# Kernel optimization log

Hardware: AMD Instinct MI355X
Metric: run time of the kernel (lower is better)

## Reference

```python
import jax, jax.numpy as jnp
import numpy as np

B, T, D = 4, 4096, 1024
H, K, V = 16, 64, 64
EPS = 1e-6


def setup_inputs() -> dict:
    key = jax.random.key(0)
    ks = jax.random.split(key, 7)
    s = 0.02
    return {
        "x": jax.random.normal(ks[0], (B, T, D), dtype=jnp.float32),
        "norm_w": jnp.ones((D,), dtype=jnp.float32),
        "Wk": jax.random.normal(ks[1], (H * K, D), dtype=jnp.float32) * s,
        "Wv": jax.random.normal(ks[2], (H * V, D), dtype=jnp.float32) * s,
        "Wo": jax.random.normal(ks[3], (D, H * V), dtype=jnp.float32) * s,
        "Wb": jax.random.normal(ks[4], (H, D), dtype=jnp.float32) * s,
        "bb": jnp.full((H,), -2.0, dtype=jnp.float32),
        "Wg": jax.random.normal(ks[5], (H, D), dtype=jnp.float32) * s,
        "bg": jnp.full((H,), 2.0, dtype=jnp.float32),
    }


def reference(x, norm_w, Wk, Wv, Wo, Wb, bb, Wg, bg):
    # RMSNorm
    rms = jnp.sqrt(jnp.mean(x * x, axis=-1, keepdims=True) + EPS)
    xn = x / rms * norm_w  # [B,T,D]

    k = (xn @ Wk.T).reshape(B, T, H, K)
    v = (xn @ Wv.T).reshape(B, T, H, V)
    # L2-normalize keys (F.normalize, eps=1e-12)
    kn = jnp.linalg.norm(k, axis=-1, keepdims=True)
    k = k / jnp.maximum(kn, 1e-12)

    beta = jax.nn.sigmoid(xn @ Wb.T + bb)  # [B,T,H]
    g = jax.nn.sigmoid(xn @ Wg.T + bg)     # [B,T,H]

    # time-major for scan
    k_t = jnp.transpose(k, (1, 0, 2, 3))       # [T,B,H,K]
    v_t = jnpp = jnp.transpose(v, (1, 0, 2, 3))  # [T,B,H,V]
    b_t = jnp.transpose(beta, (1, 0, 2))       # [T,B,H]
    g_t = jnp.transpose(g, (1, 0, 2))          # [T,B,H]

    state0 = jnp.zeros((B, H, K, V), dtype=jnp.float32)

    def step(state, inp):
        kt, vt, bt, gt = inp  # [B,H,K],[B,H,V],[B,H],[B,H]
        pred = jnp.einsum('bhkv,bhk->bhv', state, kt)
        err = vt - pred
        state = gt[..., None, None] * state + bt[..., None, None] * (kt[..., :, None] * err[..., None, :])
        out_t = jnp.einsum('bhkv,bhk->bhv', state, kt)
        return state, out_t

    final_state, out = jax.lax.scan(step, state0, (k_t, v_t, b_t, g_t))
    out = jnp.transpose(out, (1, 0, 2, 3)).reshape(B, T, H * V)  # [B,T,H*V]
    y = x + out @ Wo.T
    return y
```

## Files before the change

kernel.cpp:

```cpp
#include <hip/hip_runtime.h>
#include <stdint.h>

#define B_ 4
#define T_ 4096
#define D_ 1024
#define H_ 16
#define NPAD 2304
#define ROWS (B_*T_)

typedef __bf16 bf16x8 __attribute__((ext_vector_type(8)));
typedef float  f32x4  __attribute__((ext_vector_type(4)));
typedef unsigned short u16;
typedef u16 u16x8 __attribute__((ext_vector_type(8)));
typedef u16 u16x4 __attribute__((ext_vector_type(4)));

__device__ __forceinline__ float bf2f(u16 u){
  union { unsigned int i; float f; } x; x.i = ((unsigned int)u) << 16; return x.f;
}
__device__ __forceinline__ u16 f2bf(float f){
  union { float f; unsigned int i; } x; x.f = f;
  unsigned int r = x.i + 0x7fffu + ((x.i >> 16) & 1u);
  return (u16)(r >> 16);
}
__device__ __forceinline__ bf16x8 as_bf(u16x8 v){ union{u16x8 u; bf16x8 b;} x; x.u = v; return x.b; }

__device__ __forceinline__ void gload_lds16(const u16* g, u16* l){
  __builtin_amdgcn_global_load_lds(
      (const __attribute__((address_space(1))) unsigned int*)g,
      (__attribute__((address_space(3))) unsigned int*)l, 16, 0, 0);
}

__global__ __launch_bounds__(256) void prep_w(
    const float* __restrict__ Wk, const float* __restrict__ Wv,
    const float* __restrict__ Wb, const float* __restrict__ Wg,
    const float* __restrict__ Wo, u16* __restrict__ Wcomb, u16* __restrict__ Wob)
{
  long i = (long)blockIdx.x * 256 + threadIdx.x;
  const long tot1 = (long)NPAD * D_;
  if (i < tot1) {
    long n = i >> 10, d = i & 1023;
    float v;
    if      (n < 1024) v = Wk[n * 1024 + d];
    else if (n < 2048) v = Wv[(n - 1024) * 1024 + d];
    else if (n < 2064) v = Wb[(n - 2048) * 1024 + d];
    else if (n < 2080) v = Wg[(n - 2064) * 1024 + d];
    else               v = 0.f;
    Wcomb[i] = f2bf(v);
  } else {
    long j = i - tot1;
    Wob[j] = f2bf(Wo[j]);
  }
}

__global__ __launch_bounds__(256) void rmsnorm_k(
    const float* __restrict__ x, const float* __restrict__ w, u16* __restrict__ xn)
{
  long row = blockIdx.x;
  int tid = threadIdx.x;
  int l = tid & 63, wv = tid >> 6;
  f32x4 v = ((const f32x4*)(x + row * D_))[tid];
  float ss = v[0]*v[0] + v[1]*v[1] + v[2]*v[2] + v[3]*v[3];
  #pragma unroll
  for (int m = 1; m < 64; m <<= 1) ss += __shfl_xor(ss, m, 64);
  __shared__ float red[4];
  if (l == 0) red[wv] = ss;
  __syncthreads();
  float tot = red[0] + red[1] + red[2] + red[3];
  float inv = rsqrtf(tot * (1.f / (float)D_) + 1e-6f);
  f32x4 wv4 = ((const f32x4*)w)[tid];
  u16x4 o;
  o[0] = f2bf(v[0] * inv * wv4[0]);
  o[1] = f2bf(v[1] * inv * wv4[1]);
  o[2] = f2bf(v[2] * inv * wv4[2]);
  o[3] = f2bf(v[3] * inv * wv4[3]);
  ((u16x4*)(xn + row * D_))[tid] = o;
}

extern __shared__ f32x4 lds_dyn[];

template<int RESID, int OUTF32>
__global__ __launch_bounds__(512, 2) void gemm256(
    const u16* __restrict__ A, const u16* __restrict__ Bm,
    u16* __restrict__ Cb, float* __restrict__ Cf, const float* __restrict__ resid,
    int M, int N, int Kd)
{
  const int tid = threadIdx.x;
  const int w = tid >> 6, l = tid & 63;
  const int lm = l & 15, lq = l >> 4;
  const int wm = w >> 2, wn = w & 3;

  unsigned gx = gridDim.x;
  unsigned bid = blockIdx.y * gx + blockIdx.x;
  unsigned nwg = gx * gridDim.y;
  unsigned cpx = nwg >> 3;
  unsigned swz = (bid & 7) * cpx + (bid >> 3);
  const long bm0 = (long)(swz / gx) * 256;
  const long bn0 = (long)(swz % gx) * 256;

  char* lds = (char*)lds_dyn;

  int rowS[2], colS[2];
  #pragma unroll
  for (int r = 0; r < 2; ++r) {
    int c = r*512 + w*64 + l;
    int row = c >> 2, slot = c & 3;
    rowS[r] = row;
    colS[r] = (slot ^ (row & 3)) * 8;
  }

  auto STAGE_A = [&](int t, int q){
    char* base = lds + q*32768;
    long k0 = (long)t * 32;
    #pragma unroll
    for (int r = 0; r < 2; ++r)
      gload_lds16(A + (bm0 + rowS[r])*(long)Kd + k0 + colS[r],
                  (u16*)(base + (r*512 + w*64)*16));
  };
  auto STAGE_B = [&](int t, int q){
    char* base = lds + q*32768 + 16384;
    long k0 = (long)t * 32;
    #pragma unroll
    for (int r = 0; r < 2; ++r)
      gload_lds16(Bm + (bn0 + rowS[r])*(long)Kd + k0 + colS[r],
                  (u16*)(base + (r*512 + w*64)*16));
  };

  f32x4 acc[8][4];
  #pragma unroll
  for (int i = 0; i < 8; ++i)
    #pragma unroll
    for (int j = 0; j < 4; ++j) acc[i][j] = f32x4{0.f,0.f,0.f,0.f};

  const int NT = Kd >> 5;
  STAGE_A(0, 0); STAGE_B(0, 0);
  STAGE_A(1, 1); STAGE_B(1, 1);

  for (int t = 0; t < NT; ++t) {
    int q  = t % 3;
    int qn = (t + 2) % 3;
    int tn = (t + 2 < NT) ? (t + 2) : (NT - 1);

    asm volatile("s_waitcnt vmcnt(4)" ::: "memory");
    __builtin_amdgcn_s_barrier();
    asm volatile("" ::: "memory");

    const char* Ab = lds + q*32768;
    const char* Bb = Ab + 16384;

    bf16x8 bfr[4];
    #pragma unroll
    for (int nf = 0; nf < 4; ++nf) {
      int rr = wn*64 + nf*16 + lm;
      bfr[nf] = *(const bf16x8*)(Bb + rr*64 + (((unsigned)lq << 4) ^ ((unsigned)(rr & 3) << 4)));
    }
    bf16x8 afr[4];
    #pragma unroll
    for (int mf = 0; mf < 4; ++mf) {
      int rr = wm*128 + mf*16 + lm;
      afr[mf] = *(const bf16x8*)(Ab + rr*64 + (((unsigned)lq << 4) ^ ((unsigned)(rr & 3) << 4)));
    }
    STAGE_A(tn, qn);

    __builtin_amdgcn_s_setprio(1);
    #pragma unroll
    for (int mf = 0; mf < 4; ++mf)
      #pragma unroll
      for (int nf = 0; nf < 4; ++nf)
        acc[mf][nf] = __builtin_amdgcn_mfma_f32_16x16x32_bf16(afr[mf], bfr[nf], acc[mf][nf], 0, 0, 0);
    __builtin_amdgcn_s_setprio(0);

    __builtin_amdgcn_s_barrier();
    asm volatile("" ::: "memory");

    #pragma unroll
    for (int mf = 0; mf < 4; ++mf) {
      int rr = wm*128 + 64 + mf*16 + lm;
      afr[mf] = *(const bf16x8*)(Ab + rr*64 + (((unsigned)lq << 4) ^ ((unsigned)(rr & 3) << 4)));
    }
    STAGE_B(tn, qn);

    __builtin_amdgcn_s_setprio(1);
    #pragma unroll
    for (int mf = 0; mf < 4; ++mf)
      #pragma unroll
      for (int nf = 0; nf < 4; ++nf)
        acc[4+mf][nf] = __builtin_amdgcn_mfma_f32_16x16x32_bf16(afr[mf], bfr[nf], acc[4+mf][nf], 0, 0, 0);
    __builtin_amdgcn_s_setprio(0);
  }

  #pragma unroll
  for (int mf = 0; mf < 8; ++mf) {
    #pragma unroll
    for (int r = 0; r < 4; ++r) {
      long m = bm0 + wm*128 + mf*16 + lq*4 + r;
      #pragma unroll
      for (int nf = 0; nf < 4; ++nf) {
        long n = bn0 + wn*64 + nf*16 + lm;
        float val = acc[mf][nf][r];
        if (RESID) val += resid[m * N + n];
        if (OUTF32) Cf[m * N + n] = val;
        else        Cb[m * N + n] = f2bf(val);
      }
    }
  }
}

template<int RESID, int OUTF32>
__global__ __launch_bounds__(256) void gemm_nt(
    const u16* __restrict__ A, const u16* __restrict__ Bm,
    u16* __restrict__ Cb, float* __restrict__ Cf, const float* __restrict__ resid,
    int M, int N, int Kd)
{
  __shared__ __align__(16) u16 Als[128 * 32];
  __shared__ __align__(16) u16 Bls[128 * 32];
  const int tid = threadIdx.x;
  const int w = tid >> 6, l = tid & 63;
  const int wr = w >> 1, wc = w & 1;
  const int lm = l & 15, lq = l >> 4;

  unsigned bid = blockIdx.y * gridDim.x + blockIdx.x;
  unsigned nwg = gridDim.x * gridDim.y;
  unsigned cpx = nwg >> 3;
  unsigned swz = (bid & 7) * cpx + (bid >> 3);
  const long bm0 = (long)(swz / gridDim.x) * 128;
  const long bn0 = (long)(swz % gridDim.x) * 128;

  f32x4 zero4 = {0.f, 0.f, 0.f, 0.f};
  f32x4 acc[4][4];
  #pragma unroll
  for (int i = 0; i < 4; i++)
    #pragma unroll
    for (int j = 0; j < 4; j++) acc[i][j] = zero4;

  for (int kk = 0; kk < Kd; kk += 32) {
    __syncthreads();
    #pragma unroll
    for (int it = 0; it < 2; it++) {
      int c = tid + it * 256;
      int r = c >> 2, kb = c & 3;
      const u16* ga = A  + (bm0 + r) * Kd + kk + kb * 8;
      const u16* gb = Bm + (bn0 + r) * Kd + kk + kb * 8;
      gload_lds16(ga, Als + (it * 256 + w * 64) * 8);
      gload_lds16(gb, Bls + (it * 256 + w * 64) * 8);
    }
    __syncthreads();
    bf16x8 af[4], bfr[4];
    #pragma unroll
    for (int f = 0; f < 4; f++)
      af[f] = *(const bf16x8*)(Als + (wr * 64 + f * 16 + lm) * 32 + lq * 8);
    #pragma unroll
    for (int f = 0; f < 4; f++)
      bfr[f] = *(const bf16x8*)(Bls + (wc * 64 + f * 16 + lm) * 32 + lq * 8);
    #pragma unroll
    for (int i = 0; i < 4; i++)
      #pragma unroll
      for (int j = 0; j < 4; j++)
        acc[i][j] = __builtin_amdgcn_mfma_f32_16x16x32_bf16(af[i], bfr[j], acc[i][j], 0, 0, 0);
  }

  #pragma unroll
  for (int i = 0; i < 4; i++) {
    #pragma unroll
    for (int r = 0; r < 4; r++) {
      long m = bm0 + wr * 64 + i * 16 + lq * 4 + r;
      #pragma unroll
      for (int j = 0; j < 4; j++) {
        long n = bn0 + wc * 64 + j * 16 + lm;
        float val = acc[i][j][r];
        if (RESID) val += resid[m * N + n];
        if (OUTF32) Cf[m * N + n] = val;
        else        Cb[m * N + n] = f2bf(val);
      }
    }
  }
}

__global__ __launch_bounds__(64) void postproc(
    u16* __restrict__ kv, const float* __restrict__ bb, const float* __restrict__ bg,
    float* __restrict__ bArr, float* __restrict__ gArr)
{
  long row = blockIdx.x;
  int l = threadIdx.x;
  u16* rp = kv + row * NPAD;
  #pragma unroll
  for (int h = 0; h < 16; h++) {
    float xk = bf2f(rp[h * 64 + l]);
    float ss = xk * xk;
    #pragma unroll
    for (int m = 1; m < 64; m <<= 1) ss += __shfl_xor(ss, m, 64);
    float inv = 1.f / fmaxf(sqrtf(ss), 1e-12f);
    rp[h * 64 + l] = f2bf(xk * inv);
  }
  if (l < 32) {
    int hh = l & 15;
    float val = bf2f(rp[2048 + l]) + ((l < 16) ? bb[hh] : bg[hh]);
    float s = 1.f / (1.f + expf(-val));
    float* dst = (l < 16) ? bArr : gArr;
    long b = row >> 12;
    long t = row & 4095;
    dst[(b * H_ + hh) * (long)T_ + t] = s;
  }
}

__device__ __forceinline__ void mm64(const u16* Ab, const u16* Bb,
                                     int lm, int lq, int wr, int wc, f32x4 acc[2][2])
{
  #pragma unroll
  for (int ks = 0; ks < 2; ++ks) {
    bf16x8 af[2], bfr[2];
    #pragma unroll
    for (int mi = 0; mi < 2; ++mi)
      af[mi] = *(const bf16x8*)(Ab + (wr*32 + mi*16 + lm)*72 + ks*32 + lq*8);
    #pragma unroll
    for (int ni = 0; ni < 2; ++ni)
      bfr[ni] = *(const bf16x8*)(Bb + (wc*32 + ni*16 + lm)*72 + ks*32 + lq*8);
    #pragma unroll
    for (int mi = 0; mi < 2; ++mi)
      #pragma unroll
      for (int ni = 0; ni < 2; ++ni)
        acc[mi][ni] = __builtin_amdgcn_mfma_f32_16x16x32_bf16(af[mi], bfr[ni], acc[mi][ni], 0, 0, 0);
  }
}

__global__ __launch_bounds__(256) void chunk1(
    u16* __restrict__ kv, const float* __restrict__ bArr, const float* __restrict__ gArr,
    u16* __restrict__ p1buf, u16* __restrict__ r1buf)
{
  __shared__ __align__(16) u16 Kb[64*72];
  __shared__ __align__(16) u16 Utb[128*72];
  __shared__ __align__(16) u16 LpI[64*72];
  __shared__ __align__(16) u16 Abf[64*72];
  __shared__ __align__(16) float Ad[4*16*21];
  __shared__ float aLS[64], ainvLS[64], bLS[64], bapLS[64];
  __shared__ float aCsh;

  const int tid = threadIdx.x;
  const int w = tid >> 6, l = tid & 63;
  const int lm = l & 15, lq = l >> 4;
  const int wr = w >> 1, wc = w & 1;
  const int bh = blockIdx.x & 63, ch = blockIdx.x >> 6;
  const int b = bh >> 4, h = bh & 15;

  const u16* kbase = kv + ((long)b*T_ + ch*64)*NPAD + h*64;
  const u16* vbase = kbase + 1024;

  #pragma unroll
  for (int it = 0; it < 2; ++it) {
    int c = tid + it*256;
    int r = c >> 3, seg = (c & 7)*8;
    *(u16x8*)(Kb  + r*72 + seg) = *(const u16x8*)(kbase + (long)r*NPAD + seg);
    *(u16x8*)(Utb + r*72 + seg) = *(const u16x8*)(vbase + (long)r*NPAD + seg);
  }
  #pragma unroll
  for (int z = 0; z < 8; ++z) {
    int idx = tid + z*256;
    int rr = idx >> 5, wd = idx & 31;
    ((unsigned int*)(Utb + (64 + rr)*72))[wd] = 0u;
  }
  if (tid < 64) {
    float gv = gArr[(long)bh*T_ + ch*64 + tid];
    float bv = bArr[(long)bh*T_ + ch*64 + tid];
    float av = gv;
    #pragma unroll
    for (int off = 1; off < 64; off <<= 1) {
      float o = __shfl_up(av, off, 64);
      if (tid >= off) av *= o;
    }
    float ap = __shfl_up(av, 1, 64);
    if (tid == 0) ap = 1.f;
    float aC = __shfl(av, 63, 64);
    aLS[tid] = av; ainvLS[tid] = 1.f/av; bLS[tid] = bv; bapLS[tid] = bv*ap;
    if (tid == 0) aCsh = aC;
  }
  __syncthreads();

  f32x4 gf[2][2];
  #pragma unroll
  for (int mi = 0; mi < 2; ++mi)
    #pragma unroll
    for (int ni = 0; ni < 2; ++ni) gf[mi][ni] = f32x4{0.f,0.f,0.f,0.f};
  mm64(Kb, Kb, lm, lq, wr, wc, gf);

  float wv_[4][2][4];
  #pragma unroll
  for (int bi = 0; bi < 4; ++bi)
    #pragma unroll
    for (int ni = 0; ni < 2; ++ni) {
      int col = w*32 + ni*16 + lm;
      #pragma unroll
      for (int r = 0; r < 4; ++r) {
        int row = bi*16 + lq*4 + r;
        float sv = (col < 64) ? bf2f(Utb[row*72 + col]) : bf2f(Kb[row*72 + (col - 64)]);
        float coef = (col < 64) ? bLS[row] : bapLS[row];
        wv_[bi][ni][r] = coef * sv;
      }
    }

  #pragma unroll
  for (int mi = 0; mi < 2; ++mi)
    #pragma unroll
    for (int ni = 0; ni < 2; ++ni)
      #pragma unroll
      for (int r = 0; r < 4; ++r) {
        int row = wr*32 + mi*16 + lq*4 + r, col = wc*32 + ni*16 + lm;
        float gvl = gf[mi][ni][r];
        int rb = row >> 4, cb = col >> 4;
        Abf[row*72 + col] = f2bf((rb > cb) ? bapLS[row]*ainvLS[col]*gvl : 0.f);
        if (rb == cb)
          Ad[(rb*16 + (row & 15))*21 + (col & 15)] =
              ((col & 15) < (row & 15)) ? bapLS[row]*ainvLS[col]*gvl : 0.f;
        LpI[row*72 + col] = f2bf((col < row) ? aLS[row]*ainvLS[col]*gvl
                                             : ((col == row) ? 1.f : 0.f));
      }
  __syncthreads();

  #pragma unroll
  for (int bi = 0; bi < 4; ++bi) {
    if (bi > 0) {
      f32x4 corr[2] = { f32x4{0.f,0.f,0.f,0.f}, f32x4{0.f,0.f,0.f,0.f} };
      const int nks = (bi*16 + 31) >> 5;
      #pragma unroll
      for (int ks = 0; ks < 2; ++ks) {
        if (ks < nks) {
          bf16x8 afr = *(const bf16x8*)(Abf + (bi*16 + lm)*72 + ks*32 + lq*8);
          #pragma unroll
          for (int ni = 0; ni < 2; ++ni) {
            bf16x8 bfr = *(const bf16x8*)(Utb + (w*32 + ni*16 + lm)*72 + ks*32 + lq*8);
            corr[ni] = __builtin_amdgcn_mfma_f32_16x16x32_bf16(afr, bfr, corr[ni], 0, 0, 0);
          }
        }
      }
      #pragma unroll
      for (int ni = 0; ni < 2; ++ni)
        #pragma unroll
        for (int r = 0; r < 4; ++r) wv_[bi][ni][r] -= corr[ni][r];
    }
    #pragma unroll
    for (int i = 0; i < 16; ++i) {
      int src = ((i >> 2) << 4) | lm;
      float u0 = __shfl(wv_[bi][0][i & 3], src, 64);
      float u1 = __shfl(wv_[bi][1][i & 3], src, 64);
      #pragma unroll
      for (int r = 0; r < 4; ++r) {
        float ad = Ad[(bi*16 + lq*4 + r)*21 + i];
        wv_[bi][0][r] = fmaf(-ad, u0, wv_[bi][0][r]);
        wv_[bi][1][r] = fmaf(-ad, u1, wv_[bi][1][r]);
      }
    }
    #pragma unroll
    for (int ni = 0; ni < 2; ++ni) {
      int col = w*32 + ni*16 + lm;
      #pragma unroll
      for (int r = 0; r < 4; ++r)
        Utb[col*72 + bi*16 + lq*4 + r] = f2bf(wv_[bi][ni][r]);
    }
  }
  __syncthreads();

  const long pr_base = (((long)bh*64 + ch)*64);
  u16* qdst = kv + ((long)b*T_ + ch*64)*NPAD + h*64;
  u16* mdst = qdst + 1024;
  f32x4 acc[2][2];

  #pragma unroll
  for (int mi = 0; mi < 2; ++mi)
    #pragma unroll
    for (int ni = 0; ni < 2; ++ni) acc[mi][ni] = f32x4{0.f,0.f,0.f,0.f};
  mm64(Utb, LpI, lm, lq, wr, wc, acc);
  #pragma unroll
  for (int mi = 0; mi < 2; ++mi)
    #pragma unroll
    for (int ni = 0; ni < 2; ++ni)
      #pragma unroll
      for (int r = 0; r < 4; ++r) {
        int row = wr*32 + mi*16 + lq*4 + r, col = wc*32 + ni*16 + lm;
        p1buf[(pr_base + row)*64 + col] = f2bf(acc[mi][ni][r]);
      }

  #pragma unroll
  for (int mi = 0; mi < 2; ++mi)
    #pragma unroll
    for (int ni = 0; ni < 2; ++ni) acc[mi][ni] = f32x4{0.f,0.f,0.f,0.f};
  mm64(LpI, Utb + 64*72, lm, lq, wr, wc, acc);
  #pragma unroll
  for (int mi = 0; mi < 2; ++mi)
    #pragma unroll
    for (int ni = 0; ni < 2; ++ni)
      #pragma unroll
      for (int r = 0; r < 4; ++r) {
        int row = wr*32 + mi*16 + lq*4 + r, col = wc*32 + ni*16 + lm;
        float val = aLS[row]*bf2f(Kb[row*72 + col]) - acc[mi][ni][r];
        qdst[(long)row*NPAD + col] = f2bf(val);
      }

  {
    int kk_ = tid >> 2, sb = (tid & 3) * 16;
    float aC = aCsh;
    #pragma unroll
    for (int s5 = 0; s5 < 16; ++s5) {
      int s = sb + s5;
      Abf[kk_*72 + s] = f2bf(aC * ainvLS[s] * bf2f(Kb[s*72 + kk_]));
    }
  }
  __syncthreads();

  #pragma unroll
  for (int mi = 0; mi < 2; ++mi)
    #pragma unroll
    for (int ni = 0; ni < 2; ++ni) acc[mi][ni] = f32x4{0.f,0.f,0.f,0.f};
  mm64(Utb, Abf, lm, lq, wr, wc, acc);
  #pragma unroll
  for (int mi = 0; mi < 2; ++mi)
    #pragma unroll
    for (int ni = 0; ni < 2; ++ni)
      #pragma unroll
      for (int r = 0; r < 4; ++r) {
        int row = wr*32 + mi*16 + lq*4 + r, col = wc*32 + ni*16 + lm;
        r1buf[(pr_base + row)*64 + col] = f2bf(acc[mi][ni][r]);
      }

  #pragma unroll
  for (int mi = 0; mi < 2; ++mi)
    #pragma unroll
    for (int ni = 0; ni < 2; ++ni) acc[mi][ni] = f32x4{0.f,0.f,0.f,0.f};
  mm64(Abf, Utb + 64*72, lm, lq, wr, wc, acc);
  #pragma unroll
  for (int mi = 0; mi < 2; ++mi)
    #pragma unroll
    for (int ni = 0; ni < 2; ++ni)
      #pragma unroll
      for (int r = 0; r < 4; ++r) {
        int row = wr*32 + mi*16 + lq*4 + r, col = wc*32 + ni*16 + lm;
        float val = ((row == col) ? aCsh : 0.f) - acc[mi][ni][r];
        mdst[(long)row*NPAD + col] = f2bf(val);
      }
}

struct PF { u16x8 qf0, qf1, mf0, mf1; u16 p1[4]; u16 r1[4]; };

__global__ __launch_bounds__(256) void chunk2(
    const u16* __restrict__ kv, const u16* __restrict__ p1buf, const u16* __restrict__ r1buf,
    u16* __restrict__ outb)
{
  __shared__ __align__(16) u16 Zb[16*72];
  __shared__ __align__(16) u16 ot[64*24];
  const int tid = threadIdx.x;
  const int wcv = tid >> 6, l = tid & 63;
  const int lm = l & 15, lq = l >> 4;
  const int bh = blockIdx.x & 63, vg = blockIdx.x >> 6;
  const int b = bh >> 4, h = bh & 15;

  for (int idx = tid; idx < 16*72/2; idx += 256) ((unsigned int*)Zb)[idx] = 0u;

  const u16* pbase = p1buf + (long)bh*64*4096;
  const u16* rbase = r1buf + (long)bh*64*4096;

  auto LOADPF = [&](int ch, PF& p){
    long rq = ((long)b*T_ + ch*64 + wcv*16 + lm)*NPAD + h*64 + lq*8;
    p.qf0 = *(const u16x8*)(kv + rq);
    p.qf1 = *(const u16x8*)(kv + rq + 32);
    p.mf0 = *(const u16x8*)(kv + rq + 1024);
    p.mf1 = *(const u16x8*)(kv + rq + 1024 + 32);
    #pragma unroll
    for (int r = 0; r < 4; ++r) {
      long pv = (long)ch*4096 + (vg*16 + lq*4 + r)*64 + wcv*16 + lm;
      p.p1[r] = pbase[pv];
      p.r1[r] = rbase[pv];
    }
  };

  PF A, Bp;
  LOADPF(0, A);
  __syncthreads();

  auto STEP = [&](int ch, PF& use, PF& pre){
    bf16x8 za0 = *(const bf16x8*)(Zb + lm*72 + lq*8);
    bf16x8 za1 = *(const bf16x8*)(Zb + lm*72 + 32 + lq*8);
    if (ch < 63) LOADPF(ch + 1, pre);
    f32x4 accO = { bf2f(use.p1[0]), bf2f(use.p1[1]), bf2f(use.p1[2]), bf2f(use.p1[3]) };
    accO = __builtin_amdgcn_mfma_f32_16x16x32_bf16(za0, as_bf(use.qf0), accO, 0, 0, 0);
    accO = __builtin_amdgcn_mfma_f32_16x16x32_bf16(za1, as_bf(use.qf1), accO, 0, 0, 0);
    f32x4 accS = { bf2f(use.r1[0]), bf2f(use.r1[1]), bf2f(use.r1[2]), bf2f(use.r1[3]) };
    accS = __builtin_amdgcn_mfma_f32_16x16x32_bf16(za0, as_bf(use.mf0), accS, 0, 0, 0);
    accS = __builtin_amdgcn_mfma_f32_16x16x32_bf16(za1, as_bf(use.mf1), accS, 0, 0, 0);
    #pragma unroll
    for (int r = 0; r < 4; ++r) ot[(wcv*16 + lm)*24 + lq*4 + r] = f2bf(accO[r]);
    __syncthreads();
    #pragma unroll
    for (int r = 0; r < 4; ++r) Zb[(lq*4 + r)*72 + wcv*16 + lm] = f2bf(accS[r]);
    {
      int i2 = tid >> 2, q4 = tid & 3;
      u16x4 ov = *(const u16x4*)(ot + i2*24 + q4*4);
      *(u16x4*)(outb + ((long)b*T_ + ch*64 + i2)*D_ + h*64 + vg*16 + q4*4) = ov;
    }
    __syncthreads();
  };

  for (int c2 = 0; c2 < 32; ++c2) {
    STEP(2*c2,     A, Bp);
    STEP(2*c2 + 1, Bp, A);
  }
}

extern "C" void kernel_launch(void* const* d_in, const int* in_sizes, int n_in,
                              void* d_out, int out_size, void* d_ws, size_t ws_size,
                              hipStream_t stream) {
  const float* x     = (const float*)d_in[0];
  const float* normw = (const float*)d_in[1];
  const float* Wk    = (const float*)d_in[2];
  const float* Wv    = (const float*)d_in[3];
  const float* Wo    = (const float*)d_in[4];
  const float* Wb    = (const float*)d_in[5];
  const float* bb    = (const float*)d_in[6];
  const float* Wg    = (const float*)d_in[7];
  const float* bg    = (const float*)d_in[8];
  float* y = (float*)d_out;

  char* ws = (char*)d_ws;
  u16* xn    = (u16*)ws;   ws += (long)ROWS * D_ * 2;
  u16* Wcomb = (u16*)ws;   ws += (long)NPAD * D_ * 2;
  u16* Wob   = (u16*)ws;   ws += (long)D_ * D_ * 2;
  u16* kvb   = (u16*)ws;   ws += (long)ROWS * NPAD * 2;
  float* bA  = (float*)ws; ws += (long)B_ * H_ * T_ * 4;
  float* gA  = (float*)ws; ws += (long)B_ * H_ * T_ * 4;
  u16* outb  = (u16*)ws;   ws += (long)ROWS * D_ * 2;
  u16* r1b   = (u16*)ws;   ws += (long)64 * 64 * 4096 * 2;

  const int LDSB = 3 * 32768;
  bool big = true;
  if (hipFuncSetAttribute(reinterpret_cast<const void*>(gemm256<0,0>),
        hipFuncAttributeMaxDynamicSharedMemorySize, LDSB) != hipSuccess) big = false;
  if (hipFuncSetAttribute(reinterpret_cast<const void*>(gemm256<1,1>),
        hipFuncAttributeMaxDynamicSharedMemorySize, LDSB) != hipSuccess) big = false;

  const long prep_total = (long)NPAD * D_ + (long)D_ * D_;
  prep_w<<<dim3((unsigned)(prep_total / 256)), dim3(256), 0, stream>>>(
      Wk, Wv, Wb, Wg, Wo, Wcomb, Wob);
  rmsnorm_k<<<dim3(ROWS), dim3(256), 0, stream>>>(x, normw, xn);
  if (big)
    gemm256<0, 0><<<dim3(NPAD / 256, ROWS / 256), dim3(512), LDSB, stream>>>(
        xn, Wcomb, kvb, (float*)nullptr, (const float*)nullptr, ROWS, NPAD, D_);
  else
    gemm_nt<0, 0><<<dim3(NPAD / 128, ROWS / 128), dim3(256), 0, stream>>>(
        xn, Wcomb, kvb, (float*)nullptr, (const float*)nullptr, ROWS, NPAD, D_);
  postproc<<<dim3(ROWS), dim3(64), 0, stream>>>(kvb, bb, bg, bA, gA);
  chunk1<<<dim3(4096), dim3(256), 0, stream>>>(kvb, bA, gA, xn, r1b);
  chunk2<<<dim3(256), dim3(256), 0, stream>>>(kvb, xn, r1b, outb);
  if (big)
    gemm256<1, 1><<<dim3(D_ / 256, ROWS / 256), dim3(512), LDSB, stream>>>(
        outb, Wob, (u16*)nullptr, y, x, ROWS, D_, D_);
  else
    gemm_nt<1, 1><<<dim3(D_ / 128, ROWS / 128), dim3(256), 0, stream>>>(
        outb, Wob, (u16*)nullptr, y, x, ROWS, D_, D_);
}
```

Measured before the change: 348.8 us.

## Change LDS swizzle pattern and merge GEMM inner loop halves into one phase

The GEMM main loop now loads all 8 A fragments at once and issues both A and B prefetches before a single block of 32 MFMAs, removing the mid-iteration barrier. The LDS XOR swizzle changes to key on (row>>1)&3 instead of row&3, to cut bank conflicts on 16-byte fragment reads. This trades more live registers for fewer barriers, and the triple-buffer safety now rests on the one remaining barrier per iteration.

```diff
diff --git a/kernel.cpp b/kernel.cpp
--- a/kernel.cpp
+++ b/kernel.cpp
@@ -99,21 +99,17 @@
 
   char* lds = (char*)lds_dyn;
 
-  int rowS[2], colS[2];
-  #pragma unroll
-  for (int r = 0; r < 2; ++r) {
-    int c = r*512 + w*64 + l;
-    int row = c >> 2, slot = c & 3;
-    rowS[r] = row;
-    colS[r] = (slot ^ (row & 3)) * 8;
-  }
+  int rowS[2];
+  #pragma unroll
+  for (int r = 0; r < 2; ++r) rowS[r] = r*128 + w*16 + (l >> 2);
+  const int colS = ((l & 3) ^ ((l >> 3) & 3)) * 8;
 
   auto STAGE_A = [&](int t, int q){
     char* base = lds + q*32768;
     long k0 = (long)t * 32;
     #pragma unroll
     for (int r = 0; r < 2; ++r)
-      gload_lds16(A + (bm0 + rowS[r])*(long)Kd + k0 + colS[r],
+      gload_lds16(A + (bm0 + rowS[r])*(long)Kd + k0 + colS,
                   (u16*)(base + (r*512 + w*64)*16));
   };
   auto STAGE_B = [&](int t, int q){
@@ -121,9 +117,11 @@
     long k0 = (long)t * 32;
     #pragma unroll
     for (int r = 0; r < 2; ++r)
-      gload_lds16(Bm + (bn0 + rowS[r])*(long)Kd + k0 + colS[r],
+      gload_lds16(Bm + (bn0 + rowS[r])*(long)Kd + k0 + colS,
                   (u16*)(base + (r*512 + w*64)*16));
   };
+
+  const unsigned soff = (unsigned)(lq ^ ((lm >> 1) & 3)) << 4;
 
   f32x4 acc[8][4];
   #pragma unroll
@@ -147,44 +145,26 @@
     const char* Ab = lds + q*32768;
     const char* Bb = Ab + 16384;
 
-    bf16x8 bfr[4];
+    bf16x8 bfr[4], afr[8];
     #pragma unroll
     for (int nf = 0; nf < 4; ++nf) {
       int rr = wn*64 + nf*16 + lm;
-      bfr[nf] = *(const bf16x8*)(Bb + rr*64 + (((unsigned)lq << 4) ^ ((unsigned)(rr & 3) << 4)));
-    }
-    bf16x8 afr[4];
-    #pragma unroll
-    for (int mf = 0; mf < 4; ++mf) {
+      bfr[nf] = *(const bf16x8*)(Bb + rr*64 + soff);
+    }
+    #pragma unroll
+    for (int mf = 0; mf < 8; ++mf) {
       int rr = wm*128 + mf*16 + lm;
-      afr[mf] = *(const bf16x8*)(Ab + rr*64 + (((unsigned)lq << 4) ^ ((unsigned)(rr & 3) << 4)));
+      afr[mf] = *(const bf16x8*)(Ab + rr*64 + soff);
     }
     STAGE_A(tn, qn);
+    STAGE_B(tn, qn);
 
     __builtin_amdgcn_s_setprio(1);
     #pragma unroll
-    for (int mf = 0; mf < 4; ++mf)
+    for (int mf = 0; mf < 8; ++mf)
       #pragma unroll
       for (int nf = 0; nf < 4; ++nf)
         acc[mf][nf] = __builtin_amdgcn_mfma_f32_16x16x32_bf16(afr[mf], bfr[nf], acc[mf][nf], 0, 0, 0);
-    __builtin_amdgcn_s_setprio(0);
-
-    __builtin_amdgcn_s_barrier();
-    asm volatile("" ::: "memory");
-
-    #pragma unroll
-    for (int mf = 0; mf < 4; ++mf) {
-      int rr = wm*128 + 64 + mf*16 + lm;
-      afr[mf] = *(const bf16x8*)(Ab + rr*64 + (((unsigned)lq << 4) ^ ((unsigned)(rr & 3) << 4)));
-    }
-    STAGE_B(tn, qn);
-
-    __builtin_amdgcn_s_setprio(1);
-    #pragma unroll
-    for (int mf = 0; mf < 4; ++mf)
-      #pragma unroll
-      for (int nf = 0; nf < 4; ++nf)
-        acc[4+mf][nf] = __builtin_amdgcn_mfma_f32_16x16x32_bf16(afr[mf], bfr[nf], acc[4+mf][nf], 0, 0, 0);
     __builtin_amdgcn_s_setprio(0);
   }
 
```

Result: no change. 348.7 us (-0.0%).
